# Performance work log

Measured on AMD Instinct MI355X. Metric: run time of the kernel, lower is better.

Reference implementation:

```python
import jax, jax.numpy as jnp
import numpy as np

B, C, W = 32, 3, 512
KSIZE = 5
EPS = 8.0
ID_OFFSET = 4.0
SCALE = ID_OFFSET / (W - 1)            # identity_offset / (image_crop - 1)
DEF_OFF = (2.0 + SCALE) / 2.0          # deforming_offset
PIX_W = 2.0 / W                        # pixel width in [-1,1] coords

def _gauss_kernel2d(k):
    sigma = k * 0.15 + 0.35
    half = (k - 1) * 0.5
    x = np.linspace(-half, half, k)
    pdf = np.exp(-0.5 * (x / sigma) ** 2)
    k1 = pdf / pdf.sum()
    return np.outer(k1, k1).astype(np.float32)

def _samp_iden():
    seq = np.arange(-(W - 1), W, 2) / (W - 1.0)   # length W, identity coords
    gx = np.tile(seq, (W, 1))
    gy = gx.T
    return jnp.asarray(np.stack([gx, gy])[None].astype(np.float32))  # [1,2,W,W]

IDEN = _samp_iden()
GKER = jnp.broadcast_to(jnp.asarray(_gauss_kernel2d(KSIZE))[None, None], (2, 1, KSIZE, KSIZE))

def _blur(g):
    p = KSIZE // 2
    g = jnp.pad(g, ((0, 0), (0, 0), (p, p), (p, p)), mode='reflect')
    # depthwise conv over the 2 grid channels (groups=2)
    return jax.lax.conv_general_dilated(g, GKER, (1, 1), 'VALID', feature_group_count=2)

def _forward_grid(prim_grid):
    pg = _blur(prim_grid)
    sg = pg + IDEN                                   # prim -> samp
    # samp -> accu: conv_transpose with [1,-1] == first difference (leading zero)
    s = sg + DEF_OFF
    sx, sy = s[:, :1], s[:, 1:2]
    ax = sx - jnp.concatenate([jnp.zeros_like(sx[..., :1]), sx[..., :-1]], axis=3)
    ay = sy - jnp.concatenate([jnp.zeros_like(sy[:, :, :1]), sy[:, :, :-1]], axis=2)
    ag = jnp.concatenate([ax, ay], axis=1) / SCALE
    ag = jax.nn.relu(ag)                             # accu_clip
    # accu -> samp: conv_transpose with all-ones filter == cumulative sum
    a = ag * SCALE
    sx2 = jnp.cumsum(a[:, :1], axis=3)
    sy2 = jnp.cumsum(a[:, 1:2], axis=2)
    sg = jnp.concatenate([sx2, sy2], axis=1) - DEF_OFF
    pg = jnp.clip(sg - IDEN, -PIX_W * EPS, PIX_W * EPS)  # prim_clip
    return jnp.clip(pg + IDEN, -1.0, 1.0)                # samp_clip (hardtanh)

def _grid_sample(img, grid):
    # img [B,C,W,W], grid [B,W,W,2] in [-1,1]; bilinear, zeros padding, align_corners=True
    x = (grid[..., 0] + 1.0) * 0.5 * (W - 1)
    y = (grid[..., 1] + 1.0) * 0.5 * (W - 1)
    x0 = jnp.floor(x); y0 = jnp.floor(y)
    x1 = x0 + 1.0;     y1 = y0 + 1.0
    wx1 = x - x0; wx0 = 1.0 - wx1
    wy1 = y - y0; wy0 = 1.0 - wy1
    def gather(xi, yi):
        valid = ((xi >= 0) & (xi < W) & (yi >= 0) & (yi < W)).astype(img.dtype)
        xc = jnp.clip(xi, 0, W - 1).astype(jnp.int32)
        yc = jnp.clip(yi, 0, W - 1).astype(jnp.int32)
        v = jax.vmap(lambda im, yy, xx: im[:, yy, xx])(img, yc, xc)  # [B,C,W,W]
        return v * valid[:, None]
    return (gather(x0, y0) * (wx0 * wy0)[:, None] + gather(x1, y0) * (wx1 * wy0)[:, None]
          + gather(x0, y1) * (wx0 * wy1)[:, None] + gather(x1, y1) * (wx1 * wy1)[:, None])

def setup_inputs() -> dict:
    key = jax.random.key(0)
    k1, k2 = jax.random.split(key)
    image = jax.random.normal(k1, (B, C, W, W), dtype=jnp.float32)
    prim_grid = jax.random.normal(k2, (B, 2, W, W), dtype=jnp.float32) * 0.01
    return {"image": image, "prim_grid": prim_grid}

def reference(image, prim_grid):
    samp_grid = _forward_grid(prim_grid)
    binding_grid = jnp.transpose(samp_grid, (0, 2, 3, 1))  # [B,W,W,2]
    return _grid_sample(image, binding_grid)
```

## Files before the change

### kernel.cpp

```cpp
#include <hip/hip_runtime.h>
#include <math.h>

#define WID 512
#define NB  32
#define NC  3
#define WW  (WID * WID)

constexpr float SCALE_F   = (float)(4.0 / 511.0);
constexpr float DEF_OFF_F = (float)((2.0 + 4.0 / 511.0) * 0.5);
constexpr float CLIP_F    = 0.03125f;

__device__ __forceinline__ int refl(int r) {
  r = r < 0 ? -r : r;
  return r > WID - 1 ? 2 * (WID - 1) - r : r;
}

__device__ __forceinline__ float seqf(int i) {
  return ((float)(2 * i - 511)) / 511.0f;
}

__device__ __forceinline__ void gl_lds16(const float* g, float* l) {
  __builtin_amdgcn_global_load_lds(
      (const __attribute__((address_space(1))) void*)g,
      (__attribute__((address_space(3))) void*)l, 16, 0, 0);
}

#define KY1_ROWS 133
#define KY1_COLS 72

__global__ __launch_bounds__(512)
void grid_kernel(const float* __restrict__ pg, float* __restrict__ gridx,
                 float* __restrict__ gridy, float* __restrict__ qsum,
                 float kw0, float kw1, float kw2) {
  if (blockIdx.x < 2048) {
    const int lane = threadIdx.x & 63;
    const int wv   = threadIdx.x >> 6;
    const int R = blockIdx.x * 8 + wv;
    const int b = R >> 9;
    const int i = R & (WID - 1);
    const float* base = pg + (size_t)b * 2 * WW;

    float v[8] = {0.f,0.f,0.f,0.f,0.f,0.f,0.f,0.f};
    const int rows[5] = {refl(i - 2), refl(i - 1), i, refl(i + 1), refl(i + 2)};
    const float wts[5] = {kw0, kw1, kw2, kw1, kw0};
#pragma unroll
    for (int r = 0; r < 5; ++r) {
      const float4* p = (const float4*)(base + (size_t)rows[r] * WID + lane * 8);
      float4 A = p[0], Bq = p[1];
      float w = wts[r];
      v[0] += w * A.x;  v[1] += w * A.y;  v[2] += w * A.z;  v[3] += w * A.w;
      v[4] += w * Bq.x; v[5] += w * Bq.y; v[6] += w * Bq.z; v[7] += w * Bq.w;
    }

    float em1 = __shfl_up(v[7], 1, 64);
    float em2 = __shfl_up(v[6], 1, 64);
    float ep8 = __shfl_down(v[0], 1, 64);
    float ep9 = __shfl_down(v[1], 1, 64);
    if (lane == 0)  { em1 = v[1]; em2 = v[2]; }
    if (lane == 63) { ep8 = v[6]; ep9 = v[5]; }

    float h[8];
    h[0] = kw2 * v[0] + kw1 * (em1 + v[1]) + kw0 * (em2 + v[2]);
    h[1] = kw2 * v[1] + kw1 * (v[0] + v[2]) + kw0 * (em1 + v[3]);
#pragma unroll
    for (int k = 2; k < 6; ++k)
      h[k] = kw2 * v[k] + kw1 * (v[k - 1] + v[k + 1]) + kw0 * (v[k - 2] + v[k + 2]);
    h[6] = kw2 * v[6] + kw1 * (v[5] + v[7]) + kw0 * (v[4] + ep8);
    h[7] = kw2 * v[7] + kw1 * (v[6] + ep8) + kw0 * (v[5] + ep9);

    float s[8], a[8], p[8];
#pragma unroll
    for (int k = 0; k < 8; ++k) s[k] = h[k] + seqf(lane * 8 + k) + DEF_OFF_F;

    float sm1 = __shfl_up(s[7], 1, 64);
    if (lane == 0) sm1 = 0.0f;
    a[0] = fmaxf((s[0] - sm1) / SCALE_F, 0.0f) * SCALE_F;
#pragma unroll
    for (int k = 1; k < 8; ++k)
      a[k] = fmaxf((s[k] - s[k - 1]) / SCALE_F, 0.0f) * SCALE_F;

    p[0] = a[0];
#pragma unroll
    for (int k = 1; k < 8; ++k) p[k] = p[k - 1] + a[k];
    float incl = p[7];
#pragma unroll
    for (int off = 1; off < 64; off <<= 1) {
      float n = __shfl_up(incl, off, 64);
      if (lane >= off) incl += n;
    }
    float excl = incl - p[7];

    float og[8];
#pragma unroll
    for (int k = 0; k < 8; ++k) {
      float gx = seqf(lane * 8 + k);
      float d = (p[k] + excl) - DEF_OFF_F - gx;
      d = fminf(fmaxf(d, -CLIP_F), CLIP_F);
      og[k] = fminf(fmaxf(d + gx, -1.0f), 1.0f);
    }
    float4* o = (float4*)(gridx + ((size_t)b * WID + i) * WID + lane * 8);
    o[0] = make_float4(og[0], og[1], og[2], og[3]);
    o[1] = make_float4(og[4], og[5], og[6], og[7]);
  } else {
    const int bid  = blockIdx.x - 2048;
    const int q    = bid & 3;
    const int tile = (bid >> 2) & 7;
    const int b    = bid >> 5;
    const int q0   = q << 7;
    const int gc0  = tile << 6;

    __shared__ float L[KY1_ROWS * KY1_COLS];
    __shared__ float ss[8][64];

    const float* src = pg + ((size_t)b * 2 + 1) * WW;
    for (int idx = threadIdx.x; idx < KY1_ROWS * 18; idx += 512) {
      int lr = idx / 18;
      int k  = idx - lr * 18;
      int gr = refl(q0 - 3 + lr);
      int gcb = gc0 - 4 + (k << 2);
      gcb = gcb < 0 ? 0 : (gcb > WID - 4 ? WID - 4 : gcb);
      float4 v = *(const float4*)(src + (size_t)gr * WID + gcb);
      *(float4*)(&L[lr * KY1_COLS + (k << 2)]) = v;
    }
    __syncthreads();

    const int j   = threadIdx.x & 63;
    const int seg = threadIdx.x >> 6;

    int jcc[5];
#pragma unroll
    for (int d = 0; d < 5; ++d)
      jcc[d] = refl(gc0 + j + d - 2) - gc0 + 4;

    auto HB = [&](int r) -> float {
      const float* Lr = &L[r * KY1_COLS];
      return kw2 * Lr[jcc[2]] + kw1 * (Lr[jcc[1]] + Lr[jcc[3]])
           + kw0 * (Lr[jcc[0]] + Lr[jcc[4]]);
    };

    const int lri0 = seg * 16 + 2;
    float hm2 = HB(lri0 - 2);
    float hm1 = HB(lri0 - 1);
    float hc  = HB(lri0);
    float hp1 = HB(lri0 + 1);
    float hp2 = HB(lri0 + 2);

    const int istart = q0 + seg * 16 - 1;
    float areg[16];
    float sprev = 0.0f, suma = 0.0f;
#pragma unroll
    for (int k = 0; k <= 16; ++k) {
      float blur = kw2 * hc + kw1 * (hm1 + hp1) + kw0 * (hm2 + hp2);
      float s = blur + seqf(istart + k) + DEF_OFF_F;
      if (k == 0) {
        sprev = (q == 0 && seg == 0) ? 0.0f : s;
      } else {
        float a = fmaxf((s - sprev) / SCALE_F, 0.0f) * SCALE_F;
        areg[k - 1] = a;
        suma += a;
        sprev = s;
      }
      if (k < 16) {
        hm2 = hm1; hm1 = hc; hc = hp1; hp1 = hp2;
        hp2 = HB(lri0 + k + 3);
      }
    }

    ss[seg][j] = suma;
    __syncthreads();
    float off = 0.0f;
#pragma unroll
    for (int w = 0; w < 7; ++w)
      if (w < seg) off += ss[w][j];
    if (seg == 7)
      qsum[((size_t)b * 4 + q) * WID + gc0 + j] = off + suma;

    float* ob = gridy + (size_t)b * WW + (size_t)(q0 + seg * 16) * WID + gc0 + j;
    float cum = off;
#pragma unroll
    for (int k = 0; k < 16; ++k) {
      cum += areg[k];
      ob[(size_t)k * WID] = cum;
    }
  }
}

__global__ __launch_bounds__(128)
void ky2_kernel(float* __restrict__ gridy, const float* __restrict__ qsum) {
  const int b = blockIdx.x >> 9;
  const int i = blockIdx.x & 511;
  const int q = i >> 7;
  const int j4 = threadIdx.x << 2;
  const float* qs = qsum + (size_t)b * 4 * WID + j4;
  float ox = 0.f, oy = 0.f, oz = 0.f, ow = 0.f;
  for (int w = 0; w < q; ++w) {
    float4 t = *(const float4*)(qs + (size_t)w * WID);
    ox += t.x; oy += t.y; oz += t.z; ow += t.w;
  }
  const float gy = seqf(i);
  float* p = gridy + ((size_t)b * WID + i) * WID + j4;
  float4 v = *(float4*)p;
  auto fin = [&](float c) -> float {
    float d = c - DEF_OFF_F - gy;
    d = fminf(fmaxf(d, -CLIP_F), CLIP_F);
    return fminf(fmaxf(d + gy, -1.0f), 1.0f);
  };
  v.x = fin(v.x + ox); v.y = fin(v.y + oy);
  v.z = fin(v.z + oz); v.w = fin(v.w + ow);
  *(float4*)p = v;
}

#define STILE  16
#define SROWS  32
#define SAMP_BLOCKS (NB * NC * (WID / STILE))

template<bool FUSEY>
__global__ __launch_bounds__(1024, 8)
void sample_kernel(const float* __restrict__ img, const float* __restrict__ gridx,
                   const float* __restrict__ gridy, const float* __restrict__ qsum,
                   float* __restrict__ out) {
  const int nb = (blockIdx.x & 7) * (SAMP_BLOCKS / 8) + (blockIdx.x >> 3);
  const int rt = nb & 31;
  const int bc = nb >> 5;
  const int b  = bc / 3;
  const int c  = bc - b * 3;
  const int r0 = rt * STILE;

  __shared__ float tile[SROWS * WID];

  const float* ic = img + ((size_t)b * NC + c) * WW;
#pragma unroll
  for (int it = 0; it < 4; ++it) {
    int chunk = it * 1024 + threadIdx.x;
    int lr = chunk >> 7;
    int c4 = (chunk & 127) << 2;
    int gr = r0 - 8 + lr;
    gr = gr < 0 ? 0 : (gr > WID - 1 ? WID - 1 : gr);
    gl_lds16(ic + (size_t)gr * WID + c4, &tile[lr * WID + c4]);
  }
  __syncthreads();

  const int j    = threadIdx.x & 511;
  const int rsub = (threadIdx.x >> 9) << 3;

  float offy = 0.0f;
  if (FUSEY) {
    const int q = r0 >> 7;
    const float* qs = qsum + (size_t)b * 4 * WID + j;
    for (int w = 0; w < q; ++w) offy += qs[(size_t)w * WID];
  }

  float* ob = out + ((size_t)b * NC + c) * WW;
#pragma unroll
  for (int r = 0; r < 8; ++r) {
    const int i = r0 + rsub + r;
    const size_t gidx = ((size_t)b * WID + i) * WID + j;
    float gx = gridx[gidx];
    float gy = gridy[gidx];
    if (FUSEY) {
      const float gyl = seqf(i);
      float d = (gy + offy) - DEF_OFF_F - gyl;
      d = fminf(fmaxf(d, -CLIP_F), CLIP_F);
      gy = fminf(fmaxf(d + gyl, -1.0f), 1.0f);
    }
    float x = (gx + 1.0f) * (0.5f * (float)(WID - 1));
    float y = (gy + 1.0f) * (0.5f * (float)(WID - 1));
    float x0f = floorf(x), y0f = floorf(y);
    int x0 = (int)x0f, y0 = (int)y0f;
    float wx1 = x - x0f, wx0 = 1.0f - wx1;
    float wy1 = y - y0f, wy0 = 1.0f - wy1;
    int x1 = x0 + 1, y1 = y0 + 1;
    int x1c = x1 > WID - 1 ? WID - 1 : x1;
    int y1c = y1 > WID - 1 ? WID - 1 : y1;
    float vx1 = x1 < WID ? 1.0f : 0.0f;
    float vy1 = y1 < WID ? 1.0f : 0.0f;

    float w00 = wx0 * wy0;
    float w01 = wx1 * wy0 * vx1;
    float w10 = wx0 * wy1 * vy1;
    float w11 = wx1 * wy1 * vx1 * vy1;

    int ly0 = y0 - r0 + 8;
    int ly1 = y1c - r0 + 8;
    float v00 = tile[ly0 * WID + x0];
    float v01 = tile[ly0 * WID + x1c];
    float v10 = tile[ly1 * WID + x0];
    float v11 = tile[ly1 * WID + x1c];

    ob[(size_t)i * WID + j] = w00 * v00 + w01 * v01 + w10 * v10 + w11 * v11;
  }
}

extern "C" void kernel_launch(void* const* d_in, const int* in_sizes, int n_in,
                              void* d_out, int out_size, void* d_ws, size_t ws_size,
                              hipStream_t stream) {
  const float* img = (const float*)d_in[0];
  const float* pg  = (const float*)d_in[1];
  float* out = (float*)d_out;

  float* gridx = (float*)d_ws;
  float* gridy = gridx + (size_t)NB * WW;

  const size_t grids_bytes = (size_t)2 * NB * WW * sizeof(float);
  const size_t qsum_bytes  = (size_t)NB * 4 * WID * sizeof(float);
  const bool ws_fits = (ws_size >= grids_bytes + qsum_bytes);
  float* qsum = ws_fits ? (float*)((char*)d_ws + grids_bytes)
                        : (float*)d_out;

  double sigma = 5.0 * 0.15 + 0.35;
  double p0 = exp(-0.5 * (2.0 / sigma) * (2.0 / sigma));
  double p1 = exp(-0.5 * (1.0 / sigma) * (1.0 / sigma));
  double p2 = 1.0;
  double sum = 2.0 * p0 + 2.0 * p1 + p2;
  float kw0 = (float)(p0 / sum), kw1 = (float)(p1 / sum), kw2 = (float)(p2 / sum);

  grid_kernel<<<2048 + NB * 32, 512, 0, stream>>>(pg, gridx, gridy, qsum,
                                                  kw0, kw1, kw2);
  if (ws_fits) {
    sample_kernel<true><<<SAMP_BLOCKS, 1024, 0, stream>>>(img, gridx, gridy,
                                                          qsum, out);
  } else {
    ky2_kernel<<<NB * WID, 128, 0, stream>>>(gridy, qsum);
    sample_kernel<false><<<SAMP_BLOCKS, 1024, 0, stream>>>(img, gridx, gridy,
                                                           qsum, out);
  }
}
```

Before: 261.0 us.

## Swizzle sample tile in LDS, batch gathers, and async-load blur-y tile

The image tile in LDS is stored with an XOR swizzle of 16-byte chunks by row, so the four bilinear gathers from neighbouring rows fall on different banks. The sample loop is split into two groups of four rows, with all grid loads and LDS gathers issued before the arithmetic to raise memory-level parallelism. The edge handling is reworked with index deltas instead of validity masks. The y-blur tile load now uses direct global-to-LDS loads instead of register round trips. The main risks are extra index arithmetic, higher register pressure, and the changed clamping at the x=511 and y=511 edges.

Result: no change. 257.5 us (-1.3%).

```diff
diff --git a/kernel.cpp b/kernel.cpp
--- a/kernel.cpp
+++ b/kernel.cpp
@@ -113,14 +113,16 @@
     __shared__ float ss[8][64];
 
     const float* src = pg + ((size_t)b * 2 + 1) * WW;
-    for (int idx = threadIdx.x; idx < KY1_ROWS * 18; idx += 512) {
-      int lr = idx / 18;
-      int k  = idx - lr * 18;
-      int gr = refl(q0 - 3 + lr);
-      int gcb = gc0 - 4 + (k << 2);
-      gcb = gcb < 0 ? 0 : (gcb > WID - 4 ? WID - 4 : gcb);
-      float4 v = *(const float4*)(src + (size_t)gr * WID + gcb);
-      *(float4*)(&L[lr * KY1_COLS + (k << 2)]) = v;
+    {
+      float* lbase = &L[0];
+      for (int idx = threadIdx.x; idx < KY1_ROWS * 18; idx += 512) {
+        int lr = idx / 18;
+        int k  = idx - lr * 18;
+        int gr = refl(q0 - 3 + lr);
+        int gcb = gc0 - 4 + (k << 2);
+        gcb = gcb < 0 ? 0 : (gcb > WID - 4 ? WID - 4 : gcb);
+        gl_lds16(src + (size_t)gr * WID + gcb, lbase + (idx << 2));
+      }
     }
     __syncthreads();
 
@@ -233,10 +235,11 @@
   for (int it = 0; it < 4; ++it) {
     int chunk = it * 1024 + threadIdx.x;
     int lr = chunk >> 7;
-    int c4 = (chunk & 127) << 2;
+    int cx = chunk & 127;
+    int sc = cx ^ (lr & 7);
     int gr = r0 - 8 + lr;
     gr = gr < 0 ? 0 : (gr > WID - 1 ? WID - 1 : gr);
-    gl_lds16(ic + (size_t)gr * WID + c4, &tile[lr * WID + c4]);
+    gl_lds16(ic + (size_t)gr * WID + (sc << 2), &tile[chunk << 2]);
   }
   __syncthreads();
 
@@ -251,43 +254,63 @@
   }
 
   float* ob = out + ((size_t)b * NC + c) * WW;
-#pragma unroll
-  for (int r = 0; r < 8; ++r) {
-    const int i = r0 + rsub + r;
-    const size_t gidx = ((size_t)b * WID + i) * WID + j;
-    float gx = gridx[gidx];
-    float gy = gridy[gidx];
-    if (FUSEY) {
-      const float gyl = seqf(i);
-      float d = (gy + offy) - DEF_OFF_F - gyl;
-      d = fminf(fmaxf(d, -CLIP_F), CLIP_F);
-      gy = fminf(fmaxf(d + gyl, -1.0f), 1.0f);
-    }
-    float x = (gx + 1.0f) * (0.5f * (float)(WID - 1));
-    float y = (gy + 1.0f) * (0.5f * (float)(WID - 1));
-    float x0f = floorf(x), y0f = floorf(y);
-    int x0 = (int)x0f, y0 = (int)y0f;
-    float wx1 = x - x0f, wx0 = 1.0f - wx1;
-    float wy1 = y - y0f, wy0 = 1.0f - wy1;
-    int x1 = x0 + 1, y1 = y0 + 1;
-    int x1c = x1 > WID - 1 ? WID - 1 : x1;
-    int y1c = y1 > WID - 1 ? WID - 1 : y1;
-    float vx1 = x1 < WID ? 1.0f : 0.0f;
-    float vy1 = y1 < WID ? 1.0f : 0.0f;
-
-    float w00 = wx0 * wy0;
-    float w01 = wx1 * wy0 * vx1;
-    float w10 = wx0 * wy1 * vy1;
-    float w11 = wx1 * wy1 * vx1 * vy1;
-
-    int ly0 = y0 - r0 + 8;
-    int ly1 = y1c - r0 + 8;
-    float v00 = tile[ly0 * WID + x0];
-    float v01 = tile[ly0 * WID + x1c];
-    float v10 = tile[ly1 * WID + x0];
-    float v11 = tile[ly1 * WID + x1c];
-
-    ob[(size_t)i * WID + j] = w00 * v00 + w01 * v01 + w10 * v10 + w11 * v11;
+  const float* gxp = gridx + ((size_t)b * WID + r0 + rsub) * WID + j;
+  const float* gyp = gridy + ((size_t)b * WID + r0 + rsub) * WID + j;
+
+#pragma unroll
+  for (int half = 0; half < 2; ++half) {
+    const int ib = rsub + half * 4;
+    float gxv[4], gyv[4];
+#pragma unroll
+    for (int r = 0; r < 4; ++r) {
+      gxv[r] = gxp[(size_t)(half * 4 + r) * WID];
+      gyv[r] = gyp[(size_t)(half * 4 + r) * WID];
+    }
+    float wx0v[4], wx1v[4], wy0v[4], wy1v[4];
+    int i00[4], i01[4], i10[4], i11[4];
+#pragma unroll
+    for (int r = 0; r < 4; ++r) {
+      const int i = r0 + ib + r;
+      float gx = gxv[r];
+      float gy = gyv[r];
+      if (FUSEY) {
+        const float gyl = seqf(i);
+        float d = (gy + offy) - DEF_OFF_F - gyl;
+        d = fminf(fmaxf(d, -CLIP_F), CLIP_F);
+        gy = fminf(fmaxf(d + gyl, -1.0f), 1.0f);
+      }
+      float x = (gx + 1.0f) * (0.5f * (float)(WID - 1));
+      float y = (gy + 1.0f) * (0.5f * (float)(WID - 1));
+      float x0f = floorf(x), y0f = floorf(y);
+      int x0 = (int)x0f, y0 = (int)y0f;
+      wx1v[r] = x - x0f; wx0v[r] = 1.0f - wx1v[r];
+      wy1v[r] = y - y0f; wy0v[r] = 1.0f - wy1v[r];
+      int dx = x0 < WID - 1 ? 1 : 0;
+      int dy = y0 < WID - 1 ? 1 : 0;
+      int ly0 = y0 - r0 + 8;
+      int ly1 = ly0 + dy;
+      int k0 = (ly0 & 7) << 2;
+      int k1 = (ly1 & 7) << 2;
+      i00[r] = (ly0 << 9) + (x0 ^ k0);
+      i01[r] = (ly0 << 9) + ((x0 + dx) ^ k0);
+      i10[r] = (ly1 << 9) + (x0 ^ k1);
+      i11[r] = (ly1 << 9) + ((x0 + dx) ^ k1);
+    }
+    float v00[4], v01[4], v10[4], v11[4];
+#pragma unroll
+    for (int r = 0; r < 4; ++r) {
+      v00[r] = tile[i00[r]];
+      v01[r] = tile[i01[r]];
+      v10[r] = tile[i10[r]];
+      v11[r] = tile[i11[r]];
+    }
+#pragma unroll
+    for (int r = 0; r < 4; ++r) {
+      const int i = r0 + ib + r;
+      ob[(size_t)i * WID + j] =
+          wy0v[r] * (wx0v[r] * v00[r] + wx1v[r] * v01[r]) +
+          wy1v[r] * (wx0v[r] * v10[r] + wx1v[r] * v11[r]);
+    }
   }
 }
 
```
